# Kernel optimization log

Hardware: AMD Instinct MI355X
Metric: run time of the kernel (lower is better)

The kernel has to match this reference:

```python
import jax, jax.numpy as jnp
import numpy as np
import math

B, S, D, H, F, E, K, L, V = 1, 2048, 768, 12, 1536, 8, 2, 2, 32000


def _ln(x, w, b, eps=1e-5):
    m = x.mean(-1, keepdims=True)
    v = ((x - m) ** 2).mean(-1, keepdims=True)
    return (x - m) / jnp.sqrt(v + eps) * w + b


def setup_inputs() -> dict:
    key = jax.random.key(0)
    ks = jax.random.split(key, 16)
    std = 0.02
    inp = {
        'tokens': jax.random.randint(ks[0], (B, S), 0, V),
        'emb': jax.random.normal(ks[1], (V, D), jnp.float32) * std,
        'qkv_w': jax.random.normal(ks[2], (L, 3 * D, D), jnp.float32) * std,
        'qkv_b': jax.random.normal(ks[3], (L, 3 * D), jnp.float32) * std,
        'out_w': jax.random.normal(ks[4], (L, D, D), jnp.float32) * std,
        'out_b': jax.random.normal(ks[5], (L, D), jnp.float32) * std,
        'ln1_w': jnp.ones((L, D), jnp.float32),
        'ln1_b': jax.random.normal(ks[6], (L, D), jnp.float32) * std,
        'ln2_w': jnp.ones((L, D), jnp.float32),
        'ln2_b': jax.random.normal(ks[7], (L, D), jnp.float32) * std,
        'gate_w': jax.random.normal(ks[8], (L, E, D), jnp.float32) * std,
        'eg_w': jax.random.normal(ks[9], (L, E, F, D), jnp.float32) * std,
        'eu_w': jax.random.normal(ks[10], (L, E, F, D), jnp.float32) * std,
        'ed_w': jax.random.normal(ks[11], (L, E, D, F), jnp.float32) * std,
        'rms_w': jnp.ones((D,), jnp.float32),
    }
    return inp


def reference(tokens, emb, qkv_w, qkv_b, out_w, out_b, ln1_w, ln1_b,
              ln2_w, ln2_b, gate_w, eg_w, eu_w, ed_w, rms_w):
    Dh = D // H
    x = emb[tokens] * math.sqrt(D)  # (B,S,D)
    for l in range(L):
        # --- MultiheadAttention (batch_first, no mask, eval) ---
        qkv = x @ qkv_w[l].T + qkv_b[l]
        q, k, v = jnp.split(qkv, 3, axis=-1)
        q = q.reshape(B, S, H, Dh).transpose(0, 2, 1, 3)
        k = k.reshape(B, S, H, Dh).transpose(0, 2, 1, 3)
        v = v.reshape(B, S, H, Dh).transpose(0, 2, 1, 3)
        att = jax.nn.softmax(jnp.einsum('bhqd,bhkd->bhqk', q, k) / math.sqrt(Dh), axis=-1)
        o = jnp.einsum('bhqk,bhkd->bhqd', att, v).transpose(0, 2, 1, 3).reshape(B, S, D)
        o = o @ out_w[l].T + out_b[l]
        x = _ln(x + o, ln1_w[l], ln1_b[l])
        # --- SimpleDeepseekV3MoE: top-k gate, softmax over top-k scores ---
        gs = jnp.einsum('bsd,ed->bse', x, gate_w[l])
        topv, topi = jax.lax.top_k(gs, K)
        tw = jax.nn.softmax(topv, axis=-1)  # (B,S,K)
        # dense per-expert combine weight (0 for unselected experts)
        ew = jnp.sum(jax.nn.one_hot(topi, E, dtype=x.dtype) * tw[..., None], axis=-2)  # (B,S,E)
        hg = jax.nn.silu(jnp.einsum('bsd,efd->bsef', x, eg_w[l]))
        hu = jnp.einsum('bsd,efd->bsef', x, eu_w[l])
        ye = jnp.einsum('bsef,edf->bsed', hg * hu, ed_w[l])
        moe = jnp.einsum('bsed,bse->bsd', ye, ew)
        x = _ln(x + moe, ln2_w[l], ln2_b[l])
    # final RMSNorm (torch default eps=None -> finfo eps)
    rms = jnp.sqrt(jnp.mean(x * x, axis=-1, keepdims=True) + jnp.finfo(x.dtype).eps)
    x = x / rms * rms_w
    logits = x @ emb.T  # tied lm_head
    return logits
```

## Files before the change

### kernel.cpp

```cpp
#include <hip/hip_runtime.h>

#define SQ   2048
#define DM   768
#define NHD  12
#define DHD  64
#define FF   1536
#define NE   8
#define NL   2
#define NV   32000

typedef __attribute__((ext_vector_type(8))) short bf16x8;
typedef __attribute__((ext_vector_type(4))) float f32x4;

__device__ __forceinline__ unsigned short f2bf(float f) {
  unsigned u = __float_as_uint(f);
  return (unsigned short)((u + 0x7fffu + ((u >> 16) & 1u)) >> 16);
}
__device__ __forceinline__ float bf2f(unsigned short h) {
  return __uint_as_float(((unsigned)h) << 16);
}

#define GLD16(ldsp, gp) __builtin_amdgcn_global_load_lds( \
    (const __attribute__((address_space(1))) void*)(gp),  \
    (__attribute__((address_space(3))) void*)(ldsp), 16, 0, 0)

__global__ __launch_bounds__(256) void conv_k(const float* __restrict__ s,
    unsigned short* __restrict__ d) {
  size_t i = (size_t)(blockIdx.x * 256 + threadIdx.x) * 8;
  float4 a = *(const float4*)(s + i);
  float4 b = *(const float4*)(s + i + 4);
  int4 pk = make_int4(
      (int)((unsigned)f2bf(a.x) | ((unsigned)f2bf(a.y) << 16)),
      (int)((unsigned)f2bf(a.z) | ((unsigned)f2bf(a.w) << 16)),
      (int)((unsigned)f2bf(b.x) | ((unsigned)f2bf(b.y) << 16)),
      (int)((unsigned)f2bf(b.z) | ((unsigned)f2bf(b.w) << 16)));
  *(int4*)(d + i) = pk;
}

__global__ __launch_bounds__(256) void embed_k(const int* __restrict__ tok,
    const float* __restrict__ emb, float* __restrict__ x,
    unsigned short* __restrict__ xbf) {
  int idx = blockIdx.x * 256 + threadIdx.x;
  int s = idx / DM, d = idx % DM;
  float v = emb[(size_t)tok[s] * DM + d] * 27.712812921102035f;
  x[idx] = v;
  xbf[idx] = f2bf(v);
}

__global__ __launch_bounds__(512) void gemm256_k(
    const unsigned short* __restrict__ A, long long lda,
    const unsigned short* __restrict__ B, long long ldb,
    float* __restrict__ C, long long ldc,
    int Kd, int mT, int nT)
{
  int nwg = gridDim.x, bid = blockIdx.x;
  int q = nwg >> 3, r = nwg & 7;
  int xcd = bid & 7, j = bid >> 3;
  int wid = (xcd < r ? xcd * (q + 1) : r * (q + 1) + (xcd - r) * q) + j;
  int mt = wid % mT, nt = wid / mT;
  int m0 = mt * 128, n0 = nt * 256;
  (void)nT;

  __shared__ __align__(16) unsigned short lds[3 * 6 * 4096];

  int t = threadIdx.x, w = t >> 6, lane = t & 63;
  int wm = (w >> 2) * 64, wn = (w & 3) * 64;
  int fr = lane & 15, ksg = lane >> 4;
  int lrow = lane >> 3;
  int lchunk = ((lane & 7) ^ lrow) * 8;

  const unsigned short* sp[6];
  sp[0] = A + (size_t)(m0 +       w * 8 + lrow) * lda + lchunk;
  sp[1] = A + (size_t)(m0 +  64 + w * 8 + lrow) * lda + lchunk;
  #pragma unroll
  for (int h = 0; h < 4; ++h)
    sp[2 + h] = B + (size_t)(n0 + h * 64 + w * 8 + lrow) * ldb + lchunk;

  int rdA = (w >> 2) * 4096;
  int rdB = (2 + (w & 3)) * 4096;
  int stDst = w * 512;

  int rx = fr & 7;
  int off0 = (ksg ^ rx) * 8;
  int off1 = ((4 + ksg) ^ rx) * 8;

  int KT = Kd >> 6;
  f32x4 acc[4][4] = {};

  #pragma unroll
  for (int h = 0; h < 6; ++h)
    GLD16(&lds[h * 4096 + stDst], sp[h]);
  #pragma unroll
  for (int h = 0; h < 6; ++h)
    GLD16(&lds[(6 + h) * 4096 + stDst], sp[h] + 64);
  asm volatile("s_waitcnt vmcnt(6)" ::: "memory");
  __builtin_amdgcn_s_barrier();
  __builtin_amdgcn_sched_barrier(0);

  int buf = 0;
  for (int kt = 0; kt < KT; ++kt) {
    const unsigned short* Abl = &lds[buf * 6 * 4096 + rdA];
    const unsigned short* Bbl = &lds[buf * 6 * 4096 + rdB];
    int pf = (kt + 2 < KT);
    int pbuf = buf + 2; if (pbuf >= 3) pbuf -= 3;
    unsigned short* pd = &lds[pbuf * 6 * 4096 + stDst];
    long long koff = (long long)(kt + 2) * 64;

    if (pf) {
      GLD16(pd + 0 * 4096, sp[0] + koff);
      GLD16(pd + 1 * 4096, sp[1] + koff);
      GLD16(pd + 2 * 4096, sp[2] + koff);
    }
    {
      bf16x8 af[4], bv[4];
      #pragma unroll
      for (int m = 0; m < 4; ++m)
        af[m] = *(const bf16x8*)&Abl[(m * 16 + fr) * 64 + off0];
      #pragma unroll
      for (int n = 0; n < 4; ++n)
        bv[n] = *(const bf16x8*)&Bbl[(n * 16 + fr) * 64 + off0];
      __builtin_amdgcn_s_setprio(1);
      #pragma unroll
      for (int m = 0; m < 4; ++m)
        #pragma unroll
        for (int n = 0; n < 4; ++n)
          acc[m][n] = __builtin_amdgcn_mfma_f32_16x16x32_bf16(
              af[m], bv[n], acc[m][n], 0, 0, 0);
      __builtin_amdgcn_s_setprio(0);
    }
    if (pf) {
      GLD16(pd + 3 * 4096, sp[3] + koff);
      GLD16(pd + 4 * 4096, sp[4] + koff);
      GLD16(pd + 5 * 4096, sp[5] + koff);
    }
    {
      bf16x8 af[4], bv[4];
      #pragma unroll
      for (int m = 0; m < 4; ++m)
        af[m] = *(const bf16x8*)&Abl[(m * 16 + fr) * 64 + off1];
      #pragma unroll
      for (int n = 0; n < 4; ++n)
        bv[n] = *(const bf16x8*)&Bbl[(n * 16 + fr) * 64 + off1];
      __builtin_amdgcn_s_setprio(1);
      #pragma unroll
      for (int m = 0; m < 4; ++m)
        #pragma unroll
        for (int n = 0; n < 4; ++n)
          acc[m][n] = __builtin_amdgcn_mfma_f32_16x16x32_bf16(
              af[m], bv[n], acc[m][n], 0, 0, 0);
      __builtin_amdgcn_s_setprio(0);
    }
    if (pf) {
      asm volatile("s_waitcnt vmcnt(6)" ::: "memory");
    } else if (kt + 1 < KT) {
      asm volatile("s_waitcnt vmcnt(0)" ::: "memory");
    }
    __builtin_amdgcn_s_barrier();
    __builtin_amdgcn_sched_barrier(0);
    buf = buf + 1; if (buf == 3) buf = 0;
  }

  int rb = ksg * 4;
  #pragma unroll
  for (int m = 0; m < 4; ++m)
    #pragma unroll
    for (int n = 0; n < 4; ++n)
      #pragma unroll
      for (int rr = 0; rr < 4; ++rr)
        C[(size_t)(m0 + wm + m * 16 + rb + rr) * ldc + (n0 + wn + n * 16 + fr)] =
            acc[m][n][rr];
}

template<bool GATHER, bool BIAS, bool OBF16>
__global__ __launch_bounds__(256) void gemm_k(
    const unsigned short* __restrict__ A, long long lda, long long a_z,
    const unsigned short* __restrict__ B, long long ldb, long long b_z,
    const float* __restrict__ bias,
    void* __restrict__ C, long long ldc, long long c_z,
    int M, int N, int Kd, float scale,
    const int* __restrict__ glist, long long gl_z,
    const int* __restrict__ cnt, int mT, int nT, int Z)
{
  int nwg = gridDim.x, bid = blockIdx.x;
  int q = nwg >> 3, r = nwg & 7;
  int xcd = bid & 7, j = bid >> 3;
  int wid = (xcd < r ? xcd * (q + 1) : r * (q + 1) + (xcd - r) * q) + j;
  int z = wid % Z; int rem = wid / Z;
  int mt = rem % mT, nt = rem / mT;

  int Mz = cnt ? cnt[z] : M;
  int m0 = mt * 128, n0 = nt * 128;
  if (m0 >= Mz) return;

  const unsigned short* Ab = A + (size_t)z * a_z;
  const unsigned short* Bb = B + (size_t)z * b_z;

  __shared__ __align__(16) unsigned short As[128 * 64];
  __shared__ __align__(16) unsigned short Bs[128 * 64];

  int t = threadIdx.x, w = t >> 6, lane = t & 63;
  int wm = (w >> 1) * 64, wn = (w & 1) * 64;
  int fr = lane & 15, ksg = lane >> 4;
  int lrow = lane >> 3;
  int lchunk = ((lane & 7) ^ lrow) * 8;

  const unsigned short* ap[4];
  const unsigned short* bp[4];
  unsigned short* la[4];
  unsigned short* lb[4];
  #pragma unroll
  for (int i = 0; i < 4; ++i) {
    int rrow = w * 32 + i * 8 + lrow;
    int gr = m0 + rrow; if (gr >= Mz) gr = Mz - 1;
    int arow; if constexpr (GATHER) arow = glist[(size_t)z * gl_z + gr]; else arow = gr;
    ap[i] = Ab + (size_t)arow * lda + lchunk;
    int br = n0 + rrow; if (br >= N) br = N - 1;
    bp[i] = Bb + (size_t)br * ldb + lchunk;
    la[i] = &As[(w * 32 + i * 8) * 64];
    lb[i] = &Bs[(w * 32 + i * 8) * 64];
  }

  int rx = fr & 7;
  int off0 = ((0 + ksg) ^ rx) * 8;
  int off1 = ((4 + ksg) ^ rx) * 8;

  f32x4 acc[4][4] = {};

  for (int k0 = 0; k0 < Kd; k0 += 64) {
    #pragma unroll
    for (int i = 0; i < 4; ++i) GLD16(la[i], ap[i] + k0);
    #pragma unroll
    for (int i = 0; i < 4; ++i) GLD16(lb[i], bp[i] + k0);
    __syncthreads();
    #pragma unroll
    for (int kb = 0; kb < 2; ++kb) {
      int offk = kb ? off1 : off0;
      bf16x8 af[4], bv[4];
      #pragma unroll
      for (int m = 0; m < 4; ++m)
        af[m] = *(const bf16x8*)&As[(wm + m * 16 + fr) * 64 + offk];
      #pragma unroll
      for (int n = 0; n < 4; ++n)
        bv[n] = *(const bf16x8*)&Bs[(wn + n * 16 + fr) * 64 + offk];
      #pragma unroll
      for (int m = 0; m < 4; ++m)
        #pragma unroll
        for (int n = 0; n < 4; ++n)
          acc[m][n] = __builtin_amdgcn_mfma_f32_16x16x32_bf16(
              af[m], bv[n], acc[m][n], 0, 0, 0);
    }
    __syncthreads();
  }

  int rb = ksg * 4;
  #pragma unroll
  for (int m = 0; m < 4; ++m) {
    #pragma unroll
    for (int n = 0; n < 4; ++n) {
      int col = n0 + wn + n * 16 + fr;
      if (col >= N) continue;
      #pragma unroll
      for (int rr = 0; rr < 4; ++rr) {
        int row = m0 + wm + m * 16 + rb + rr;
        if (row >= Mz) continue;
        float v = acc[m][n][rr] * scale;
        if constexpr (BIAS) v += bias[col];
        size_t off = (size_t)z * c_z + (size_t)row * ldc + col;
        if constexpr (OBF16) ((unsigned short*)C)[off] = f2bf(v);
        else                 ((float*)C)[off] = v;
      }
    }
  }
}

__global__ __launch_bounds__(256) void transpose_v_k(
    const unsigned short* __restrict__ qkv, unsigned short* __restrict__ vt) {
  int kt = blockIdx.x;
  int h  = blockIdx.y;
  __shared__ unsigned short tile[64][72];
  int t = threadIdx.x;
  int r = t >> 2;
  int c0 = (t & 3) * 16;
  const unsigned short* src =
      qkv + (size_t)(kt * 64 + r) * (3 * DM) + 2 * DM + h * DHD + c0;
  *(int4*)&tile[r][c0]     = *(const int4*)(src);
  *(int4*)&tile[r][c0 + 8] = *(const int4*)(src + 8);
  __syncthreads();
  unsigned u[8];
  #pragma unroll
  for (int j = 0; j < 8; ++j)
    u[j] = (unsigned)tile[c0 + 2 * j][r] | ((unsigned)tile[c0 + 2 * j + 1][r] << 16);
  unsigned short* dst = vt + (size_t)(h * DHD + r) * SQ + kt * 64 + c0;
  *(int4*)dst       = make_int4((int)u[0], (int)u[1], (int)u[2], (int)u[3]);
  *(int4*)(dst + 8) = make_int4((int)u[4], (int)u[5], (int)u[6], (int)u[7]);
}

__global__ __launch_bounds__(256) void flash_k(
    const unsigned short* __restrict__ qkv,
    const unsigned short* __restrict__ vt,
    unsigned short* __restrict__ o)
{
  int nwg = gridDim.x, bid = blockIdx.x;
  int cpx = nwg >> 3;
  int wid = (bid & 7) * cpx + (bid >> 3);
  int h  = wid >> 5;
  int qt = wid & 31;
  int q0 = qt * 64;

  __shared__ __align__(16) unsigned short Ks[128 * 64];
  __shared__ __align__(16) unsigned short Vs[128 * 64];
  __shared__ __align__(16) unsigned short Ps[4][16 * 136];

  int t = threadIdx.x, w = t >> 6, lane = t & 63;
  int fr = lane & 15, ksg = lane >> 4;
  int lrow = lane >> 3;
  int lchunk = ((lane & 7) ^ lrow) * 8;

  const unsigned short* qbase = qkv + (size_t)q0 * (3 * DM) + h * DHD;
  #pragma unroll
  for (int i = 0; i < 2; ++i) {
    int rrow = w * 16 + i * 8 + lrow;
    GLD16(&Ks[(w * 16 + i * 8) * 64], qbase + (size_t)rrow * (3 * DM) + lchunk);
  }
  __syncthreads();
  bf16x8 qf[2];
  {
    int row = w * 16 + fr, ph = fr & 7;
    qf[0] = *(const bf16x8*)&Ks[row * 64 + ((ksg ^ ph) * 8)];
    qf[1] = *(const bf16x8*)&Ks[row * 64 + (((4 + ksg) ^ ph) * 8)];
  }
  __syncthreads();

  const unsigned short* kbase = qkv + DM + h * DHD;
  const unsigned short* vb = vt + (size_t)(h * DHD) * SQ;

  f32x4 oacc[4] = {};
  float m_r[4] = {-1e30f, -1e30f, -1e30f, -1e30f};
  float l_r[4] = {0.f, 0.f, 0.f, 0.f};

  for (int kt = 0; kt < SQ / 128; ++kt) {
    int kk0 = kt * 128;
    #pragma unroll
    for (int i = 0; i < 4; ++i) {
      int rrow = w * 32 + i * 8 + lrow;
      GLD16(&Ks[(w * 32 + i * 8) * 64],
            kbase + (size_t)(kk0 + rrow) * (3 * DM) + lchunk);
    }
    #pragma unroll
    for (int i = 0; i < 4; ++i) {
      int p = w * 32 + i * 8 + lrow;
      GLD16(&Vs[(w * 32 + i * 8) * 64],
            vb + (size_t)(p >> 1) * SQ + kk0 + (p & 1) * 64 + lchunk);
    }
    __syncthreads();

    f32x4 sacc[8] = {};
    #pragma unroll
    for (int kb = 0; kb < 2; ++kb) {
      #pragma unroll
      for (int n = 0; n < 8; ++n) {
        int row = n * 16 + fr;
        bf16x8 bvv = *(const bf16x8*)&Ks[row * 64 +
            (((kb * 4 + ksg) ^ (fr & 7)) * 8)];
        sacc[n] = __builtin_amdgcn_mfma_f32_16x16x32_bf16(
            qf[kb], bvv, sacc[n], 0, 0, 0);
      }
    }

    #pragma unroll
    for (int r = 0; r < 4; ++r) {
      float mx = sacc[0][r];
      #pragma unroll
      for (int n = 1; n < 8; ++n) mx = fmaxf(mx, sacc[n][r]);
      mx = fmaxf(mx, __shfl_xor(mx, 1));
      mx = fmaxf(mx, __shfl_xor(mx, 2));
      mx = fmaxf(mx, __shfl_xor(mx, 4));
      mx = fmaxf(mx, __shfl_xor(mx, 8));
      float mn = fmaxf(m_r[r], mx * 0.125f);
      float resc = __expf(m_r[r] - mn);
      m_r[r] = mn;
      #pragma unroll
      for (int n = 0; n < 4; ++n) oacc[n][r] *= resc;
      float rs = 0.f;
      #pragma unroll
      for (int n = 0; n < 8; ++n) {
        float p = __expf(sacc[n][r] * 0.125f - mn);
        rs += p;
        Ps[w][(ksg * 4 + r) * 136 + n * 16 + fr] = f2bf(p);
      }
      rs += __shfl_xor(rs, 1);
      rs += __shfl_xor(rs, 2);
      rs += __shfl_xor(rs, 4);
      rs += __shfl_xor(rs, 8);
      l_r[r] = l_r[r] * resc + rs;
    }

    #pragma unroll
    for (int ksi = 0; ksi < 4; ++ksi) {
      bf16x8 pa = *(const bf16x8*)&Ps[w][fr * 136 + ksi * 32 + ksg * 8];
      #pragma unroll
      for (int n = 0; n < 4; ++n) {
        int p = (n * 16 + fr) * 2 + (ksi >> 1);
        int c = (ksi & 1) * 4 + ksg;
        bf16x8 bvv = *(const bf16x8*)&Vs[p * 64 + ((c ^ (p & 7)) * 8)];
        oacc[n] = __builtin_amdgcn_mfma_f32_16x16x32_bf16(
            pa, bvv, oacc[n], 0, 0, 0);
      }
    }
    __syncthreads();
  }

  unsigned short* ob = o + (size_t)(q0 + w * 16) * DM + h * DHD;
  #pragma unroll
  for (int r = 0; r < 4; ++r) {
    float invl = 1.f / l_r[r];
    int qrow = ksg * 4 + r;
    #pragma unroll
    for (int n = 0; n < 4; ++n)
      ob[(size_t)qrow * DM + n * 16 + fr] = f2bf(oacc[n][r] * invl);
  }
}

__global__ __launch_bounds__(256) void add_ln_k(const float* __restrict__ xin,
    const float* __restrict__ add, const float* __restrict__ w,
    const float* __restrict__ b, float* __restrict__ xout,
    unsigned short* __restrict__ xbf) {
  int row = blockIdx.x, t = threadIdx.x;
  const float* xi = xin + (size_t)row * DM;
  const float* ai = add + (size_t)row * DM;
  float v[3]; float s = 0.f, sq = 0.f;
  #pragma unroll
  for (int i = 0; i < 3; ++i) {
    int idx = t + i * 256;
    v[i] = xi[idx] + ai[idx];
    s += v[i]; sq += v[i] * v[i];
  }
  #pragma unroll
  for (int o = 32; o; o >>= 1) { s += __shfl_xor(s, o); sq += __shfl_xor(sq, o); }
  __shared__ float rsm[4], rqm[4];
  int wv = t >> 6;
  if ((t & 63) == 0) { rsm[wv] = s; rqm[wv] = sq; }
  __syncthreads();
  s = rsm[0] + rsm[1] + rsm[2] + rsm[3];
  sq = rqm[0] + rqm[1] + rqm[2] + rqm[3];
  float mean = s * (1.f / 768.f);
  float var = sq * (1.f / 768.f) - mean * mean;
  float inv = rsqrtf(var + 1e-5f);
  float* xo = xout + (size_t)row * DM;
  unsigned short* xb = xbf + (size_t)row * DM;
  #pragma unroll
  for (int i = 0; i < 3; ++i) {
    int idx = t + i * 256;
    float y = (v[i] - mean) * inv * w[idx] + b[idx];
    xo[idx] = y; xb[idx] = f2bf(y);
  }
}

__global__ void gate_topk_k(const float* __restrict__ x, const float* __restrict__ gw,
    float* __restrict__ tw, int* __restrict__ ti, int* __restrict__ cnt,
    int* __restrict__ lists, int* __restrict__ slot) {
  int sIdx = blockIdx.x, lane = threadIdx.x;
  const float* xr = x + (size_t)sIdx * DM;
  float acc[NE] = {};
  for (int d = lane; d < DM; d += 64) {
    float xv = xr[d];
    #pragma unroll
    for (int e = 0; e < NE; ++e) acc[e] += xv * gw[e * DM + d];
  }
  #pragma unroll
  for (int e = 0; e < NE; ++e) {
    #pragma unroll
    for (int o = 32; o; o >>= 1) acc[e] += __shfl_down(acc[e], o);
  }
  if (lane == 0) {
    float v0 = -1e30f, v1 = -1e30f; int i0 = 0, i1 = 0;
    #pragma unroll
    for (int e = 0; e < NE; ++e) {
      float v = acc[e];
      if (v > v0) { v1 = v0; i1 = i0; v0 = v; i0 = e; }
      else if (v > v1) { v1 = v; i1 = e; }
    }
    float e1 = expf(v1 - v0);
    float inv = 1.f / (1.f + e1);
    tw[sIdx * 2] = inv; tw[sIdx * 2 + 1] = e1 * inv;
    ti[sIdx * 2] = i0;  ti[sIdx * 2 + 1] = i1;
    int p0 = atomicAdd(&cnt[i0], 1); lists[i0 * SQ + p0] = sIdx; slot[sIdx * 2] = p0;
    int p1 = atomicAdd(&cnt[i1], 1); lists[i1 * SQ + p1] = sIdx; slot[sIdx * 2 + 1] = p1;
  }
}

__global__ void zero_k(int* __restrict__ c) {
  if (threadIdx.x < NE) c[threadIdx.x] = 0;
}

__global__ __launch_bounds__(256) void silu_mul_k(unsigned short* __restrict__ hg,
    const unsigned short* __restrict__ hu, const int* __restrict__ cnt) {
  int e = blockIdx.y, sl = blockIdx.x;
  if (sl >= cnt[e]) return;
  size_t base = ((size_t)e * SQ + sl) * FF;
  int t = threadIdx.x;
  #pragma unroll
  for (int i = 0; i < FF / 256; ++i) {
    size_t idx = base + t + i * 256;
    float g = bf2f(hg[idx]);
    float u = bf2f(hu[idx]);
    float sv = g / (1.f + expf(-g));
    hg[idx] = f2bf(sv * u);
  }
}

__global__ __launch_bounds__(256) void combine_ln_k(const float* __restrict__ xin,
    const float* __restrict__ ye, const float* __restrict__ tw,
    const int* __restrict__ ti, const int* __restrict__ slot,
    const float* __restrict__ w, const float* __restrict__ b,
    float* __restrict__ xout, unsigned short* __restrict__ xbf) {
  int row = blockIdx.x, t = threadIdx.x;
  int e0 = ti[row * 2], e1 = ti[row * 2 + 1];
  int p0 = slot[row * 2], p1 = slot[row * 2 + 1];
  float w0 = tw[row * 2], w1 = tw[row * 2 + 1];
  const float* y0 = ye + ((size_t)e0 * SQ + p0) * DM;
  const float* y1 = ye + ((size_t)e1 * SQ + p1) * DM;
  const float* xi = xin + (size_t)row * DM;
  float v[3]; float s = 0.f, sq = 0.f;
  #pragma unroll
  for (int i = 0; i < 3; ++i) {
    int idx = t + i * 256;
    v[i] = xi[idx] + w0 * y0[idx] + w1 * y1[idx];
    s += v[i]; sq += v[i] * v[i];
  }
  #pragma unroll
  for (int o = 32; o; o >>= 1) { s += __shfl_xor(s, o); sq += __shfl_xor(sq, o); }
  __shared__ float rsm[4], rqm[4];
  int wv = t >> 6;
  if ((t & 63) == 0) { rsm[wv] = s; rqm[wv] = sq; }
  __syncthreads();
  s = rsm[0] + rsm[1] + rsm[2] + rsm[3];
  sq = rqm[0] + rqm[1] + rqm[2] + rqm[3];
  float mean = s * (1.f / 768.f);
  float var = sq * (1.f / 768.f) - mean * mean;
  float inv = rsqrtf(var + 1e-5f);
  float* xo = xout + (size_t)row * DM;
  unsigned short* xb = xbf + (size_t)row * DM;
  #pragma unroll
  for (int i = 0; i < 3; ++i) {
    int idx = t + i * 256;
    float y = (v[i] - mean) * inv * w[idx] + b[idx];
    xo[idx] = y; xb[idx] = f2bf(y);
  }
}

__global__ __launch_bounds__(256) void rms_k(const float* __restrict__ x,
    const float* __restrict__ rw, unsigned short* __restrict__ xbf) {
  int row = blockIdx.x, t = threadIdx.x;
  const float* xi = x + (size_t)row * DM;
  float v[3]; float sq = 0.f;
  #pragma unroll
  for (int i = 0; i < 3; ++i) {
    int idx = t + i * 256;
    v[i] = xi[idx];
    sq += v[i] * v[i];
  }
  #pragma unroll
  for (int o = 32; o; o >>= 1) sq += __shfl_xor(sq, o);
  __shared__ float rqm[4];
  int wv = t >> 6;
  if ((t & 63) == 0) rqm[wv] = sq;
  __syncthreads();
  sq = rqm[0] + rqm[1] + rqm[2] + rqm[3];
  float inv = rsqrtf(sq * (1.f / 768.f) + 1.1920929e-07f);
  unsigned short* xb = xbf + (size_t)row * DM;
  #pragma unroll
  for (int i = 0; i < 3; ++i) {
    int idx = t + i * 256;
    xb[idx] = f2bf(v[i] * inv * rw[idx]);
  }
}

extern "C" void kernel_launch(void* const* d_in, const int* in_sizes, int n_in,
                              void* d_out, int out_size, void* d_ws, size_t ws_size,
                              hipStream_t stream) {
  (void)in_sizes; (void)n_in; (void)out_size; (void)ws_size;
  const int*   tokens = (const int*)d_in[0];
  const float* emb    = (const float*)d_in[1];
  const float* qkv_w  = (const float*)d_in[2];
  const float* qkv_b  = (const float*)d_in[3];
  const float* out_w  = (const float*)d_in[4];
  const float* out_b  = (const float*)d_in[5];
  const float* ln1_w  = (const float*)d_in[6];
  const float* ln1_b  = (const float*)d_in[7];
  const float* ln2_w  = (const float*)d_in[8];
  const float* ln2_b  = (const float*)d_in[9];
  const float* gate_w = (const float*)d_in[10];
  const float* eg_w   = (const float*)d_in[11];
  const float* eu_w   = (const float*)d_in[12];
  const float* ed_w   = (const float*)d_in[13];
  const float* rms_w  = (const float*)d_in[14];
  float* out = (float*)d_out;

  char* wsb = (char*)d_ws;
  float*          x_f    = (float*)(wsb + 0);
  unsigned short* x_bf   = (unsigned short*)(wsb + 6291456);
  unsigned short* qkv_bf = (unsigned short*)(wsb + 9437184);
  unsigned short* vt     = (unsigned short*)(wsb + 18874368);
  unsigned short* o_bf   = (unsigned short*)(wsb + 22020096);
  float*          tmp_f  = (float*)(wsb + 25165824);
  float*          tw     = (float*)(wsb + 31457280);
  int*            ti     = (int*)(wsb + 31473664);
  int*            cnt    = (int*)(wsb + 31490048);
  int*            lists  = (int*)(wsb + 31490304);
  int*            slot   = (int*)(wsb + 31555840);
  unsigned short* emb_bf = (unsigned short*)(wsb + 31572224);
  unsigned short* wbf    = (unsigned short*)(wsb + 80724224);
  unsigned short* hg     = (unsigned short*)(wsb + 142065920);
  unsigned short* hu     = (unsigned short*)(wsb + 142065920 + 50331648);
  float*          ye     = (float*)(wsb + 142065920 + 50331648);

  unsigned short* qw_bf = wbf;
  unsigned short* ow_bf = wbf + 1769472;
  unsigned short* eg_bf = wbf + 2359296;
  unsigned short* eu_bf = wbf + 11796480;
  unsigned short* ed_bf = wbf + 21233664;

  conv_k<<<12000, 256, 0, stream>>>(emb, emb_bf);
  embed_k<<<SQ * DM / 256, 256, 0, stream>>>(tokens, emb, x_f, x_bf);

  for (int l = 0; l < NL; ++l) {
    const float* qw = qkv_w + (size_t)l * 3 * DM * DM;
    const float* qb = qkv_b + (size_t)l * 3 * DM;
    const float* ow = out_w + (size_t)l * DM * DM;
    const float* ob = out_b + (size_t)l * DM;
    const float* gw = gate_w + (size_t)l * NE * DM;
    const float* egw = eg_w + (size_t)l * NE * FF * DM;
    const float* euw = eu_w + (size_t)l * NE * FF * DM;
    const float* edw = ed_w + (size_t)l * NE * DM * FF;

    conv_k<<<864, 256, 0, stream>>>(qw, qw_bf);
    conv_k<<<288, 256, 0, stream>>>(ow, ow_bf);
    conv_k<<<4608, 256, 0, stream>>>(egw, eg_bf);
    conv_k<<<4608, 256, 0, stream>>>(euw, eu_bf);
    conv_k<<<4608, 256, 0, stream>>>(edw, ed_bf);

    gemm_k<false, true, true><<<16 * 18, 256, 0, stream>>>(
        x_bf, DM, 0, qw_bf, DM, 0, qb, qkv_bf, 3 * DM, 0,
        SQ, 3 * DM, DM, 1.f, nullptr, 0, nullptr, 16, 18, 1);

    transpose_v_k<<<dim3(SQ / 64, NHD), 256, 0, stream>>>(qkv_bf, vt);

    flash_k<<<NHD * 32, 256, 0, stream>>>(qkv_bf, vt, o_bf);

    gemm_k<false, true, false><<<16 * 6, 256, 0, stream>>>(
        o_bf, DM, 0, ow_bf, DM, 0, ob, tmp_f, DM, 0,
        SQ, DM, DM, 1.f, nullptr, 0, nullptr, 16, 6, 1);

    add_ln_k<<<SQ, 256, 0, stream>>>(x_f, tmp_f, ln1_w + l * DM, ln1_b + l * DM,
                                     x_f, x_bf);

    zero_k<<<1, 64, 0, stream>>>(cnt);
    gate_topk_k<<<SQ, 64, 0, stream>>>(x_f, gw, tw, ti, cnt, lists, slot);

    gemm_k<true, false, true><<<16 * 12 * NE, 256, 0, stream>>>(
        x_bf, DM, 0, eg_bf, DM, (long long)FF * DM, nullptr,
        hg, FF, (long long)SQ * FF,
        SQ, FF, DM, 1.f, lists, SQ, cnt, 16, 12, NE);
    gemm_k<true, false, true><<<16 * 12 * NE, 256, 0, stream>>>(
        x_bf, DM, 0, eu_bf, DM, (long long)FF * DM, nullptr,
        hu, FF, (long long)SQ * FF,
        SQ, FF, DM, 1.f, lists, SQ, cnt, 16, 12, NE);

    silu_mul_k<<<dim3(SQ, NE), 256, 0, stream>>>(hg, hu, cnt);

    gemm_k<false, false, false><<<16 * 6 * NE, 256, 0, stream>>>(
        hg, FF, (long long)SQ * FF, ed_bf, FF, (long long)DM * FF, nullptr,
        ye, DM, (long long)SQ * DM,
        SQ, DM, FF, 1.f, nullptr, 0, cnt, 16, 6, NE);

    combine_ln_k<<<SQ, 256, 0, stream>>>(x_f, ye, tw, ti, slot,
                                         ln2_w + l * DM, ln2_b + l * DM,
                                         x_f, x_bf);
  }

  rms_k<<<SQ, 256, 0, stream>>>(x_f, rms_w, x_bf);

  gemm256_k<<<16 * 125, 512, 0, stream>>>(
      x_bf, DM, emb_bf, DM, out, NV, DM, 16, 125);
}
```

Baseline: 834.3 us.

## Fuse expert gate/up GEMMs into big-tile kernel, batch weight conversions, shrink flash blocks

Generalizes the 128x256 big-tile GEMM with gathered rows, a per-expert batch index and bf16 output. The separate gate and up expert GEMMs become one launch over 16 batch slots, relying on eu_bf sitting right after eg_bf in the workspace so z indexes both. Per-layer fp32-to-bf16 weight conversions are merged into two launches, and flash attention now uses 128-thread blocks with 32 query rows each, doubling the block count. The aim is fewer launches, better MFMA tile efficiency for the expert GEMMs and more parallelism in attention, at the cost of wasted work on padded expert tiles and more K/V reloads per query.

```diff
diff --git a/kernel.cpp b/kernel.cpp
--- a/kernel.cpp
+++ b/kernel.cpp
@@ -24,17 +24,42 @@
     (const __attribute__((address_space(1))) void*)(gp),  \
     (__attribute__((address_space(3))) void*)(ldsp), 16, 0, 0)
 
-__global__ __launch_bounds__(256) void conv_k(const float* __restrict__ s,
-    unsigned short* __restrict__ d) {
-  size_t i = (size_t)(blockIdx.x * 256 + threadIdx.x) * 8;
-  float4 a = *(const float4*)(s + i);
-  float4 b = *(const float4*)(s + i + 4);
+__device__ __forceinline__ void conv8(const float* s, unsigned short* d) {
+  float4 a = *(const float4*)s;
+  float4 b = *(const float4*)(s + 4);
   int4 pk = make_int4(
       (int)((unsigned)f2bf(a.x) | ((unsigned)f2bf(a.y) << 16)),
       (int)((unsigned)f2bf(a.z) | ((unsigned)f2bf(a.w) << 16)),
       (int)((unsigned)f2bf(b.x) | ((unsigned)f2bf(b.y) << 16)),
       (int)((unsigned)f2bf(b.z) | ((unsigned)f2bf(b.w) << 16)));
-  *(int4*)(d + i) = pk;
+  *(int4*)d = pk;
+}
+
+__global__ __launch_bounds__(256) void conv_k(const float* __restrict__ s,
+    unsigned short* __restrict__ d) {
+  size_t i = (size_t)(blockIdx.x * 256 + threadIdx.x) * 8;
+  conv8(s + i, d + i);
+}
+
+__global__ __launch_bounds__(256) void conv3_k(const float* __restrict__ s0,
+    const float* __restrict__ s1, const float* __restrict__ s2,
+    unsigned short* __restrict__ d, int per) {
+  int b = blockIdx.x;
+  const float* s = (b < per) ? s0 : (b < 2 * per) ? s1 : s2;
+  int sb = (b < per) ? b : (b < 2 * per) ? b - per : b - 2 * per;
+  size_t di = (size_t)b * 2048 + threadIdx.x * 8;
+  size_t si = (size_t)sb * 2048 + threadIdx.x * 8;
+  conv8(s + si, d + di);
+}
+
+__global__ __launch_bounds__(256) void conv2_k(const float* __restrict__ s0,
+    const float* __restrict__ s1, unsigned short* __restrict__ d, int per0) {
+  int b = blockIdx.x;
+  const float* s = (b < per0) ? s0 : s1;
+  int sb = (b < per0) ? b : b - per0;
+  size_t di = (size_t)b * 2048 + threadIdx.x * 8;
+  size_t si = (size_t)sb * 2048 + threadIdx.x * 8;
+  conv8(s + si, d + di);
 }
 
 __global__ __launch_bounds__(256) void embed_k(const int* __restrict__ tok,
@@ -47,19 +72,28 @@
   xbf[idx] = f2bf(v);
 }
 
+template<bool GATHER, bool OBF16>
 __global__ __launch_bounds__(512) void gemm256_k(
     const unsigned short* __restrict__ A, long long lda,
-    const unsigned short* __restrict__ B, long long ldb,
-    float* __restrict__ C, long long ldc,
-    int Kd, int mT, int nT)
+    const unsigned short* __restrict__ B, long long ldb, long long b_z,
+    void* __restrict__ C, long long ldc, long long c_z,
+    int M, int Kd, int mT, int nT, int Z, int zmod,
+    const int* __restrict__ glist, long long gl_z,
+    const int* __restrict__ cnt)
 {
   int nwg = gridDim.x, bid = blockIdx.x;
   int q = nwg >> 3, r = nwg & 7;
   int xcd = bid & 7, j = bid >> 3;
   int wid = (xcd < r ? xcd * (q + 1) : r * (q + 1) + (xcd - r) * q) + j;
-  int mt = wid % mT, nt = wid / mT;
+  int z = wid % Z; int rem = wid / Z;
+  int mt = rem % mT, nt = rem / mT;
+  int zz = z % zmod;
+  int Mz = cnt ? cnt[zz] : M;
   int m0 = mt * 128, n0 = nt * 256;
+  if (m0 >= Mz) return;
   (void)nT;
+
+  const unsigned short* Bz = B + (size_t)z * b_z;
 
   __shared__ __align__(16) unsigned short lds[3 * 6 * 4096];
 
@@ -70,11 +104,16 @@
   int lchunk = ((lane & 7) ^ lrow) * 8;
 
   const unsigned short* sp[6];
-  sp[0] = A + (size_t)(m0 +       w * 8 + lrow) * lda + lchunk;
-  sp[1] = A + (size_t)(m0 +  64 + w * 8 + lrow) * lda + lchunk;
-  #pragma unroll
-  for (int h = 0; h < 4; ++h)
-    sp[2 + h] = B + (size_t)(n0 + h * 64 + w * 8 + lrow) * ldb + lchunk;
+  #pragma unroll
+  for (int hh = 0; hh < 2; ++hh) {
+    int gr = m0 + hh * 64 + w * 8 + lrow; if (gr >= Mz) gr = Mz - 1;
+    int arow;
+    if constexpr (GATHER) arow = glist[(size_t)zz * gl_z + gr]; else arow = gr;
+    sp[hh] = A + (size_t)arow * lda + lchunk;
+  }
+  #pragma unroll
+  for (int hh = 0; hh < 4; ++hh)
+    sp[2 + hh] = Bz + (size_t)(n0 + hh * 64 + w * 8 + lrow) * ldb + lchunk;
 
   int rdA = (w >> 2) * 4096;
   int rdB = (2 + (w & 3)) * 4096;
@@ -162,13 +201,20 @@
 
   int rb = ksg * 4;
   #pragma unroll
-  for (int m = 0; m < 4; ++m)
-    #pragma unroll
-    for (int n = 0; n < 4; ++n)
-      #pragma unroll
-      for (int rr = 0; rr < 4; ++rr)
-        C[(size_t)(m0 + wm + m * 16 + rb + rr) * ldc + (n0 + wn + n * 16 + fr)] =
-            acc[m][n][rr];
+  for (int m = 0; m < 4; ++m) {
+    #pragma unroll
+    for (int n = 0; n < 4; ++n) {
+      #pragma unroll
+      for (int rr = 0; rr < 4; ++rr) {
+        int row = m0 + wm + m * 16 + rb + rr;
+        if (row >= Mz) continue;
+        size_t off = (size_t)z * c_z + (size_t)row * ldc +
+                     (n0 + wn + n * 16 + fr);
+        if constexpr (OBF16) ((unsigned short*)C)[off] = f2bf(acc[m][n][rr]);
+        else                 ((float*)C)[off] = acc[m][n][rr];
+      }
+    }
+  }
 }
 
 template<bool GATHER, bool BIAS, bool OBF16>
@@ -295,7 +341,7 @@
   *(int4*)(dst + 8) = make_int4((int)u[4], (int)u[5], (int)u[6], (int)u[7]);
 }
 
-__global__ __launch_bounds__(256) void flash_k(
+__global__ __launch_bounds__(128) void flash_k(
     const unsigned short* __restrict__ qkv,
     const unsigned short* __restrict__ vt,
     unsigned short* __restrict__ o)
@@ -303,13 +349,13 @@
   int nwg = gridDim.x, bid = blockIdx.x;
   int cpx = nwg >> 3;
   int wid = (bid & 7) * cpx + (bid >> 3);
-  int h  = wid >> 5;
-  int qt = wid & 31;
-  int q0 = qt * 64;
+  int h  = wid >> 6;
+  int qt = wid & 63;
+  int q0 = qt * 32;
 
   __shared__ __align__(16) unsigned short Ks[128 * 64];
   __shared__ __align__(16) unsigned short Vs[128 * 64];
-  __shared__ __align__(16) unsigned short Ps[4][16 * 136];
+  __shared__ __align__(16) unsigned short Ps[2][16 * 136];
 
   int t = threadIdx.x, w = t >> 6, lane = t & 63;
   int fr = lane & 15, ksg = lane >> 4;
@@ -341,15 +387,15 @@
   for (int kt = 0; kt < SQ / 128; ++kt) {
     int kk0 = kt * 128;
     #pragma unroll
-    for (int i = 0; i < 4; ++i) {
-      int rrow = w * 32 + i * 8 + lrow;
-      GLD16(&Ks[(w * 32 + i * 8) * 64],
+    for (int i = 0; i < 8; ++i) {
+      int rrow = w * 64 + i * 8 + lrow;
+      GLD16(&Ks[(w * 64 + i * 8) * 64],
             kbase + (size_t)(kk0 + rrow) * (3 * DM) + lchunk);
     }
     #pragma unroll
-    for (int i = 0; i < 4; ++i) {
-      int p = w * 32 + i * 8 + lrow;
-      GLD16(&Vs[(w * 32 + i * 8) * 64],
+    for (int i = 0; i < 8; ++i) {
+      int p = w * 64 + i * 8 + lrow;
+      GLD16(&Vs[(w * 64 + i * 8) * 64],
             vb + (size_t)(p >> 1) * SQ + kk0 + (p & 1) * 64 + lchunk);
     }
     __syncthreads();
@@ -627,18 +673,15 @@
   for (int l = 0; l < NL; ++l) {
     const float* qw = qkv_w + (size_t)l * 3 * DM * DM;
     const float* qb = qkv_b + (size_t)l * 3 * DM;
+    const float* ob = out_b + (size_t)l * DM;
     const float* ow = out_w + (size_t)l * DM * DM;
-    const float* ob = out_b + (size_t)l * DM;
     const float* gw = gate_w + (size_t)l * NE * DM;
     const float* egw = eg_w + (size_t)l * NE * FF * DM;
     const float* euw = eu_w + (size_t)l * NE * FF * DM;
     const float* edw = ed_w + (size_t)l * NE * DM * FF;
 
-    conv_k<<<864, 256, 0, stream>>>(qw, qw_bf);
-    conv_k<<<288, 256, 0, stream>>>(ow, ow_bf);
-    conv_k<<<4608, 256, 0, stream>>>(egw, eg_bf);
-    conv_k<<<4608, 256, 0, stream>>>(euw, eu_bf);
-    conv_k<<<4608, 256, 0, stream>>>(edw, ed_bf);
+    conv2_k<<<1152, 256, 0, stream>>>(qw, ow, qw_bf, 864);
+    conv3_k<<<13824, 256, 0, stream>>>(egw, euw, edw, eg_bf, 4608);
 
     gemm_k<false, true, true><<<16 * 18, 256, 0, stream>>>(
         x_bf, DM, 0, qw_bf, DM, 0, qb, qkv_bf, 3 * DM, 0,
@@ -646,7 +689,7 @@
 
     transpose_v_k<<<dim3(SQ / 64, NHD), 256, 0, stream>>>(qkv_bf, vt);
 
-    flash_k<<<NHD * 32, 256, 0, stream>>>(qkv_bf, vt, o_bf);
+    flash_k<<<NHD * 64, 128, 0, stream>>>(qkv_bf, vt, o_bf);
 
     gemm_k<false, true, false><<<16 * 6, 256, 0, stream>>>(
         o_bf, DM, 0, ow_bf, DM, 0, ob, tmp_f, DM, 0,
@@ -658,14 +701,10 @@
     zero_k<<<1, 64, 0, stream>>>(cnt);
     gate_topk_k<<<SQ, 64, 0, stream>>>(x_f, gw, tw, ti, cnt, lists, slot);
 
-    gemm_k<true, false, true><<<16 * 12 * NE, 256, 0, stream>>>(
-        x_bf, DM, 0, eg_bf, DM, (long long)FF * DM, nullptr,
+    gemm256_k<true, true><<<16 * 6 * 16, 512, 0, stream>>>(
+        x_bf, DM, eg_bf, DM, (long long)FF * DM,
         hg, FF, (long long)SQ * FF,
-        SQ, FF, DM, 1.f, lists, SQ, cnt, 16, 12, NE);
-    gemm_k<true, false, true><<<16 * 12 * NE, 256, 0, stream>>>(
-        x_bf, DM, 0, eu_bf, DM, (long long)FF * DM, nullptr,
-        hu, FF, (long long)SQ * FF,
-        SQ, FF, DM, 1.f, lists, SQ, cnt, 16, 12, NE);
+        SQ, DM, 16, 6, 16, 8, lists, SQ, cnt);
 
     silu_mul_k<<<dim3(SQ, NE), 256, 0, stream>>>(hg, hu, cnt);
 
@@ -681,6 +720,7 @@
 
   rms_k<<<SQ, 256, 0, stream>>>(x_f, rms_w, x_bf);
 
-  gemm256_k<<<16 * 125, 512, 0, stream>>>(
-      x_bf, DM, emb_bf, DM, out, NV, DM, 16, 125);
-}
+  gemm256_k<false, false><<<16 * 125, 512, 0, stream>>>(
+      x_bf, DM, emb_bf, DM, 0, out, NV, 0,
+      SQ, DM, 16, 125, 1, 1, nullptr, 0, nullptr);
+}
```

Measured after the change: 813.1 us. -2.5%, faster.
